# Kernel optimization log

Hardware: AMD Instinct MI355X
Metric: run time of the kernel (lower is better)

## Reference

```python
import jax, jax.numpy as jnp
import numpy as np

EMBED_DIM = 512
NUM_HEADS = 8
HEAD_DIM = EMBED_DIM // NUM_HEADS
SCALING = HEAD_DIM ** -0.5
T, B = 2048, 4
NEG_INF = -1e9


def setup_inputs() -> dict:
    key = jax.random.key(0)
    k1, k2, k3 = jax.random.split(key, 3)
    h = jax.random.normal(k1, (T, B, EMBED_DIM), dtype=jnp.float32)
    # causal additive mask, [T, T]: 0 on/below diagonal, -inf above
    attn_mask = jnp.where(jnp.triu(jnp.ones((T, T), dtype=bool), k=1), NEG_INF, 0.0).astype(jnp.float32)
    in_proj_weight = jax.random.normal(k2, (3 * EMBED_DIM, EMBED_DIM), dtype=jnp.float32) * 0.02
    in_proj_bias = jnp.zeros((3 * EMBED_DIM,), dtype=jnp.float32)
    out_w = jax.random.normal(k3, (EMBED_DIM, EMBED_DIM), dtype=jnp.float32) * 0.02
    out_b = jnp.zeros((EMBED_DIM,), dtype=jnp.float32)
    return {"h": h, "attn_mask": attn_mask, "in_proj_weight": in_proj_weight,
            "in_proj_bias": in_proj_bias, "out_w": out_w, "out_b": out_b}


def reference(h, attn_mask, in_proj_weight, in_proj_bias, out_w, out_b):
    tgt_len, bsz, embed_dim = h.shape
    # fused QKV projection: [T, B, 3E]
    qkv = jnp.einsum('tbe,fe->tbf', h, in_proj_weight) + in_proj_bias
    q, k, v = jnp.split(qkv, 3, axis=-1)
    q = q * SCALING
    # [T, B, E] -> [B*H, T, hd]
    def to_heads(x):
        return x.reshape(tgt_len, bsz * NUM_HEADS, HEAD_DIM).transpose(1, 0, 2)
    q, k, v = to_heads(q), to_heads(k), to_heads(v)
    # scores: [B*H, T, S]
    attn_weights = jnp.einsum('bth,bsh->bts', q, k)
    attn_weights = attn_weights + attn_mask[None, :, :]
    attn_p = jax.nn.softmax(attn_weights, axis=-1)
    attn = jnp.einsum('bts,bsh->bth', attn_p, v)
    # [B*H, T, hd] -> [T, B, E]
    attn = attn.transpose(1, 0, 2).reshape(tgt_len, bsz, embed_dim)
    out = jnp.einsum('tbe,fe->tbf', attn, out_w) + out_b
    return out, attn_p.reshape(bsz, NUM_HEADS, tgt_len, tgt_len)
```

## Files before the change

kernel.cpp:

```cpp
#include <hip/hip_runtime.h>
#include <cstdint>
#include <cstddef>

#define T_SEQ 2048
#define BSZ 4
#define EMB 512
#define NH 8
#define HD 64
#define SCALING 0.125f
#define NEGBIG (-1e30f)
#define PW 144

typedef short bf16x8_t __attribute__((ext_vector_type(8)));
typedef float f32x4_t __attribute__((ext_vector_type(4)));
typedef short short4v __attribute__((ext_vector_type(4)));
typedef float float4v __attribute__((ext_vector_type(4)));

typedef __attribute__((address_space(1))) const void* as1_cvp;
typedef __attribute__((address_space(3))) void* as3_vp;

#define MFMA16(a, b, c) __builtin_amdgcn_mfma_f32_16x16x32_bf16((a), (b), (c), 0, 0, 0)

static __device__ __forceinline__ short f2b(float f) {
  union { float f; uint32_t u; } x; x.f = f;
  uint32_t r = (x.u + 0x7fffu + ((x.u >> 16) & 1u)) >> 16;
  return (short)(r & 0xffffu);
}

static __device__ __forceinline__ void gload_lds16(const void* g, void* l) {
  __builtin_amdgcn_global_load_lds((as1_cvp)g, (as3_vp)l, 16, 0, 0);
}

__global__ __launch_bounds__(256) void cvt_kernel(const float* __restrict__ in,
                                                  short* __restrict__ out) {
  int i = (blockIdx.x * 256 + threadIdx.x) * 4;
  float4v v = *(const float4v*)(in + i);
  short4v o;
  o[0] = f2b(v[0]); o[1] = f2b(v[1]); o[2] = f2b(v[2]); o[3] = f2b(v[3]);
  *(short4v*)(out + i) = o;
}

template <int EPI>
__global__ __launch_bounds__(256)
void gemm_bt(const short* __restrict__ A, const short* __restrict__ Bt,
             const float* __restrict__ bias,
             short* __restrict__ outQ, short* __restrict__ outK, short* __restrict__ outV,
             float* __restrict__ outF, float* __restrict__ Pfill) {
  __shared__ short ldsA[128 * 32];
  __shared__ short ldsB[128 * 32];
  const int tid = threadIdx.x;
  const int wid = tid >> 6, lane = tid & 63, g = lane >> 4, r16 = lane & 15;
  const int wr = wid >> 1, wc = wid & 1;
  const int mbase = blockIdx.y * 128, nbase = blockIdx.x * 128;

  f32x4_t acc[4][4];
#pragma unroll
  for (int m = 0; m < 4; ++m)
#pragma unroll
    for (int n = 0; n < 4; ++n) acc[m][n] = (f32x4_t){0.f, 0.f, 0.f, 0.f};

  for (int kt = 0; kt < 16; ++kt) {
    __syncthreads();
#pragma unroll
    for (int i = 0; i < 2; ++i) {
      int c = i * 256 + tid;
      int row = c >> 2, j4 = c & 3;
      gload_lds16(A + (size_t)(mbase + row) * 512 + kt * 32 + j4 * 8, &ldsA[c * 8]);
      gload_lds16(Bt + (size_t)(nbase + row) * 512 + kt * 32 + j4 * 8, &ldsB[c * 8]);
    }
    __syncthreads();
    bf16x8_t af[4], bfv[4];
#pragma unroll
    for (int m = 0; m < 4; ++m)
      af[m] = *(const bf16x8_t*)&ldsA[(wr * 64 + m * 16 + r16) * 32 + g * 8];
#pragma unroll
    for (int n = 0; n < 4; ++n)
      bfv[n] = *(const bf16x8_t*)&ldsB[(wc * 64 + n * 16 + r16) * 32 + g * 8];
#pragma unroll
    for (int m = 0; m < 4; ++m)
#pragma unroll
      for (int n = 0; n < 4; ++n) acc[m][n] = MFMA16(af[m], bfv[n], acc[m][n]);
  }

#pragma unroll
  for (int m = 0; m < 4; ++m) {
#pragma unroll
    for (int n = 0; n < 4; ++n) {
      int col = nbase + wc * 64 + n * 16 + r16;
      float bcol = bias[col];
#pragma unroll
      for (int j = 0; j < 4; ++j) {
        int row = mbase + wr * 64 + m * 16 + g * 4 + j;
        float v = acc[m][n][j] + bcol;
        if (EPI == 0) {
          int sect = col >> 9, e = col & 511, hh = e >> 6, d = e & 63;
          int t = row >> 2, b = row & 3;
          size_t dst = ((size_t)(b * NH + hh) * T_SEQ + t) * HD + d;
          short bv = f2b(v);
          if (sect == 0) outQ[dst] = bv;
          else if (sect == 1) outK[dst] = bv;
          else outV[dst] = bv;
        } else {
          outF[(size_t)row * EMB + col] = v;
        }
      }
    }
  }

  if (EPI == 0) {
    const int bid = blockIdx.y * gridDim.x + blockIdx.x;
    const int nblk = gridDim.x * gridDim.y;
    const float4v z = {0.f, 0.f, 0.f, 0.f};
    for (int pair = bid; pair < 1024; pair += nblk) {
      const int qt = pair >> 5, bh = pair & 31;
      const int c0 = (qt + 1) * 64;
      const int nf4 = (T_SEQ - c0) >> 2;
      if (nf4 <= 0) continue;
      float* base = Pfill + ((size_t)bh * T_SEQ + qt * 64) * T_SEQ + c0;
      for (int r = 0; r < 64; ++r) {
        float* rowp = base + (size_t)r * T_SEQ;
        for (int c = tid; c < nf4; c += 256)
          __builtin_nontemporal_store(z, (float4v*)(rowp + c * 4));
      }
    }
  }
}

__global__ __launch_bounds__(256)
void attn_fused(const short* __restrict__ Qg, const short* __restrict__ Kg,
                const short* __restrict__ Vg, float* __restrict__ Pout,
                short* __restrict__ attnO) {
  __shared__ __align__(16) short lds[26624];
  short* Kt = lds;
  short* Vt = lds + 8192;
  short(*Pl)[16 * PW] = (short(*)[16 * PW])(lds + 8192 + 9216);
  const int bh = blockIdx.x;
  const int qt = 31 - (int)blockIdx.y;
  const int tid = threadIdx.x, wid = tid >> 6, lane = tid & 63;
  const int g = lane >> 4, r16 = lane & 15;
  const size_t headOff = (size_t)bh * T_SEQ * HD;
  const int wrow0 = qt * 64 + wid * 16;
  const int myrow = wrow0 + r16;
  const int maxcol = qt * 64 + 64;
  const int nt128 = (qt >> 1) + 1;
  const short* Kh = Kg + headOff;
  const short* Vh = Vg + headOff;

  bf16x8_t qf[2];
  {
    const short* qp = Qg + headOff + (size_t)myrow * HD + g * 8;
    qf[0] = *(const bf16x8_t*)qp;
    qf[1] = *(const bf16x8_t*)(qp + 32);
  }

  float m_w = NEGBIG;
  float m_t = NEGBIG;
  float l_w = 0.f;
  f32x4_t oacc[4];
#pragma unroll
  for (int dc = 0; dc < 4; ++dc) oacc[dc] = (f32x4_t){0.f, 0.f, 0.f, 0.f};

  uint32_t* Vtu = (uint32_t*)Vt;
  const int kp0 = tid & 63, dg0 = tid >> 6;

  bf16x8_t va[2], vb[2];
#define VLOAD(KB)                                                              \
  {                                                                            \
    const short* vp0 = Vh + (size_t)((KB) + kp0 * 2) * HD + dg0 * 8;           \
    va[0] = *(const bf16x8_t*)vp0; vb[0] = *(const bf16x8_t*)(vp0 + HD);       \
    const short* vp1 = vp0 + 32;                                               \
    va[1] = *(const bf16x8_t*)vp1; vb[1] = *(const bf16x8_t*)(vp1 + HD);       \
  }
  VLOAD(0)

  for (int kt = 0; kt < nt128; ++kt) {
    const int kb = kt * 128;
    __syncthreads();
#pragma unroll
    for (int i = 0; i < 4; ++i) {
      int cc = i * 256 + tid;
      int row = cc >> 3, j8 = (cc & 7) ^ (row & 7);
      gload_lds16(Kh + (size_t)(kb + row) * HD + j8 * 8, &Kt[cc * 8]);
    }
#pragma unroll
    for (int i = 0; i < 2; ++i) {
      int dg = dg0 + i * 4;
#pragma unroll
      for (int j = 0; j < 8; ++j)
        Vtu[(dg * 8 + j) * (PW / 2) + kp0] =
            (uint32_t)(uint16_t)va[i][j] | ((uint32_t)(uint16_t)vb[i][j] << 16);
    }
    __syncthreads();
    if (kt + 1 < nt128) VLOAD(kb + 128)
    const int H = ((maxcol - kb) >= 128) ? 2 : 1;
#pragma unroll
    for (int h = 0; h < 2; ++h) {
      if (h < H) {
        float sv[4][4];
#pragma unroll
        for (int kc4 = 0; kc4 < 4; ++kc4) {
          const int rl = (h * 4 + kc4) * 16 + r16;
          f32x4_t s = {0.f, 0.f, 0.f, 0.f};
#pragma unroll
          for (int kk = 0; kk < 2; ++kk) {
            int byteo = (rl * 128 + kk * 64 + g * 16) ^ ((rl & 7) << 4);
            bf16x8_t kf = *(const bf16x8_t*)((const char*)Kt + byteo);
            s = MFMA16(kf, qf[kk], s);
          }
          const int key0 = kb + (h * 4 + kc4) * 16 + g * 4;
#pragma unroll
          for (int j = 0; j < 4; ++j)
            sv[kc4][j] = (key0 + j <= myrow) ? s[j] * SCALING : NEGBIG;
        }
        float pm = NEGBIG;
#pragma unroll
        for (int kc4 = 0; kc4 < 4; ++kc4)
#pragma unroll
          for (int j = 0; j < 4; ++j) pm = fmaxf(pm, sv[kc4][j]);
        m_t = fmaxf(m_t, pm);
#pragma unroll
        for (int off = 1; off < 64; off <<= 1) pm = fmaxf(pm, __shfl_xor(pm, off));
        float mn = fmaxf(m_w, pm);
        if (mn > m_w + 8.f) {
          float sc = __expf(m_w - mn);
          l_w *= sc;
#pragma unroll
          for (int dc = 0; dc < 4; ++dc)
#pragma unroll
            for (int j = 0; j < 4; ++j) oacc[dc][j] *= sc;
          m_w = mn;
        }
#pragma unroll
        for (int kc4 = 0; kc4 < 4; ++kc4) {
          short4v pb;
#pragma unroll
          for (int j = 0; j < 4; ++j) {
            float e = __expf(sv[kc4][j] - m_w);
            l_w += e;
            pb[j] = f2b(e);
          }
          *(short4v*)&Pl[wid][r16 * PW + (h * 4 + kc4) * 16 + g * 4] = pb;
        }
#pragma unroll
        for (int kk2 = 0; kk2 < 2; ++kk2) {
          const int kc2 = h * 2 + kk2;
          bf16x8_t pf = *(const bf16x8_t*)&Pl[wid][r16 * PW + kc2 * 32 + g * 8];
#pragma unroll
          for (int dc = 0; dc < 4; ++dc) {
            bf16x8_t vf = *(const bf16x8_t*)&Vt[(dc * 16 + r16) * PW + kc2 * 32 + g * 8];
            oacc[dc] = MFMA16(pf, vf, oacc[dc]);
          }
        }
      }
    }
  }

#pragma unroll
  for (int off = 16; off <= 32; off <<= 1) {
    m_t = fmaxf(m_t, __shfl_xor(m_t, off));
    l_w += __shfl_xor(l_w, off);
  }
  const float m_row = m_t;
  const float rl2 = __expf(m_row - m_w) / l_w;

  float lo[4];
#pragma unroll
  for (int j = 0; j < 4; ++j) lo[j] = 1.0f / __shfl(l_w, g * 4 + j);
#pragma unroll
  for (int dc = 0; dc < 4; ++dc) {
#pragma unroll
    for (int j = 0; j < 4; ++j) {
      int t = wrow0 + g * 4 + j, d = dc * 16 + r16;
      size_t ntok = (size_t)t * BSZ + (bh >> 3);
      attnO[ntok * EMB + (bh & 7) * HD + d] = f2b(oacc[dc][j] * lo[j]);
    }
  }

  short* Kb0 = lds;
  short* Kb1 = lds + 8192;
  float* Prow = Pout + ((size_t)bh * T_SEQ + myrow) * T_SEQ;

#define STAGEK(KB, BUF)                                                        \
  {                                                                            \
    _Pragma("unroll")                                                          \
    for (int i = 0; i < 4; ++i) {                                              \
      int cc = i * 256 + tid;                                                  \
      int row = cc >> 3, j8 = (cc & 7) ^ (row & 7);                            \
      gload_lds16(Kh + (size_t)((KB) + row) * HD + j8 * 8, &(BUF)[cc * 8]);    \
    }                                                                          \
  }

  __syncthreads();
  STAGEK(0, Kb0)
  __syncthreads();
  int p = 0;
  for (int kt = 0; kt < nt128; ++kt) {
    const int kb = kt * 128;
    short* cur = p ? Kb1 : Kb0;
    short* nxt = p ? Kb0 : Kb1;
    if (kt + 1 < nt128) STAGEK(kb + 128, nxt)
    const int navail = (maxcol - kb) >> 4;
    const int nkc = navail < 8 ? navail : 8;
#pragma unroll
    for (int kc = 0; kc < 8; ++kc) {
      if (kc < nkc) {
        const int rl = kc * 16 + r16;
        f32x4_t s = {0.f, 0.f, 0.f, 0.f};
#pragma unroll
        for (int kk = 0; kk < 2; ++kk) {
          int byteo = (rl * 128 + kk * 64 + g * 16) ^ ((rl & 7) << 4);
          bf16x8_t kf = *(const bf16x8_t*)((const char*)cur + byteo);
          s = MFMA16(kf, qf[kk], s);
        }
        const int key0 = kb + kc * 16 + g * 4;
        float4v pvv;
#pragma unroll
        for (int j = 0; j < 4; ++j) {
          float e = __expf(s[j] * SCALING - m_row) * rl2;
          pvv[j] = (key0 + j <= myrow) ? e : 0.f;
        }
        *(float4v*)(Prow + key0) = pvv;
      }
    }
    __syncthreads();
    p ^= 1;
  }
}

extern "C" void kernel_launch(void* const* d_in, const int* in_sizes, int n_in,
                              void* d_out, int out_size, void* d_ws, size_t ws_size,
                              hipStream_t stream) {
  const float* h = (const float*)d_in[0];
  const float* w_in = (const float*)d_in[2];
  const float* b_in = (const float*)d_in[3];
  const float* w_out = (const float*)d_in[4];
  const float* b_out = (const float*)d_in[5];
  float* out = (float*)d_out;
  float* Pout = out + (size_t)T_SEQ * BSZ * EMB;

  short* hB = (short*)d_ws;
  short* wB = hB + (size_t)8192 * 512;
  short* owB = wB + (size_t)1536 * 512;
  short* qB = owB + (size_t)512 * 512;
  short* kB = qB + (size_t)32 * 2048 * 64;
  short* vB = kB + (size_t)32 * 2048 * 64;
  short* aB = vB + (size_t)32 * 2048 * 64;

  cvt_kernel<<<4096, 256, 0, stream>>>(h, hB);
  cvt_kernel<<<768, 256, 0, stream>>>(w_in, wB);
  cvt_kernel<<<256, 256, 0, stream>>>(w_out, owB);

  gemm_bt<0><<<dim3(12, 64), 256, 0, stream>>>(hB, wB, b_in, qB, kB, vB, nullptr, Pout);
  attn_fused<<<dim3(32, 32), 256, 0, stream>>>(qB, kB, vB, Pout, aB);
  gemm_bt<1><<<dim3(4, 64), 256, 0, stream>>>(aB, owB, b_out, nullptr, nullptr, nullptr, out, nullptr);
}
```

Measured before the change: 233.8 us.

## Write unnormalized probabilities in first pass and rescale instead of recomputing scores

The second pass that recomputed QK^T from restaged K tiles is removed. The first pass now writes the unnormalized exp values straight to the probability output and records the running max for each 64-key chunk in shared memory. A final pass reads P back from global memory and rescales each chunk by exp(m_chunk - m_final)/l. This drops the K staging and score MFMAs of the second pass, but adds a full read and rewrite of the large fp32 P matrix, so whether it pays off depends on how much of that traffic stays in cache.

```diff
diff --git a/kernel.cpp b/kernel.cpp
--- a/kernel.cpp
+++ b/kernel.cpp
@@ -134,6 +134,7 @@
   short* Kt = lds;
   short* Vt = lds + 8192;
   short(*Pl)[16 * PW] = (short(*)[16 * PW])(lds + 8192 + 9216);
+  __shared__ float mwt[4][32];
   const int bh = blockIdx.x;
   const int qt = 31 - (int)blockIdx.y;
   const int tid = threadIdx.x, wid = tid >> 6, lane = tid & 63;
@@ -145,6 +146,7 @@
   const int nt128 = (qt >> 1) + 1;
   const short* Kh = Kg + headOff;
   const short* Vh = Vg + headOff;
+  float* Prow = Pout + ((size_t)bh * T_SEQ + myrow) * T_SEQ;
 
   bf16x8_t qf[2];
   {
@@ -154,7 +156,6 @@
   }
 
   float m_w = NEGBIG;
-  float m_t = NEGBIG;
   float l_w = 0.f;
   f32x4_t oacc[4];
 #pragma unroll
@@ -217,7 +218,6 @@
         for (int kc4 = 0; kc4 < 4; ++kc4)
 #pragma unroll
           for (int j = 0; j < 4; ++j) pm = fmaxf(pm, sv[kc4][j]);
-        m_t = fmaxf(m_t, pm);
 #pragma unroll
         for (int off = 1; off < 64; off <<= 1) pm = fmaxf(pm, __shfl_xor(pm, off));
         float mn = fmaxf(m_w, pm);
@@ -230,15 +230,20 @@
             for (int j = 0; j < 4; ++j) oacc[dc][j] *= sc;
           m_w = mn;
         }
+        if (lane == 0) mwt[wid][kt * 2 + h] = m_w;
 #pragma unroll
         for (int kc4 = 0; kc4 < 4; ++kc4) {
+          const int key0 = kb + (h * 4 + kc4) * 16 + g * 4;
           short4v pb;
+          float4v ev;
 #pragma unroll
           for (int j = 0; j < 4; ++j) {
             float e = __expf(sv[kc4][j] - m_w);
             l_w += e;
+            ev[j] = e;
             pb[j] = f2b(e);
           }
+          *(float4v*)(Prow + key0) = ev;
           *(short4v*)&Pl[wid][r16 * PW + (h * 4 + kc4) * 16 + g * 4] = pb;
         }
 #pragma unroll
@@ -256,12 +261,7 @@
   }
 
 #pragma unroll
-  for (int off = 16; off <= 32; off <<= 1) {
-    m_t = fmaxf(m_t, __shfl_xor(m_t, off));
-    l_w += __shfl_xor(l_w, off);
-  }
-  const float m_row = m_t;
-  const float rl2 = __expf(m_row - m_w) / l_w;
+  for (int off = 16; off <= 32; off <<= 1) l_w += __shfl_xor(l_w, off);
 
   float lo[4];
 #pragma unroll
@@ -276,54 +276,18 @@
     }
   }
 
-  short* Kb0 = lds;
-  short* Kb1 = lds + 8192;
-  float* Prow = Pout + ((size_t)bh * T_SEQ + myrow) * T_SEQ;
-
-#define STAGEK(KB, BUF)                                                        \
-  {                                                                            \
-    _Pragma("unroll")                                                          \
-    for (int i = 0; i < 4; ++i) {                                              \
-      int cc = i * 256 + tid;                                                  \
-      int row = cc >> 3, j8 = (cc & 7) ^ (row & 7);                            \
-      gload_lds16(Kh + (size_t)((KB) + row) * HD + j8 * 8, &(BUF)[cc * 8]);    \
-    }                                                                          \
-  }
-
-  __syncthreads();
-  STAGEK(0, Kb0)
-  __syncthreads();
-  int p = 0;
-  for (int kt = 0; kt < nt128; ++kt) {
-    const int kb = kt * 128;
-    short* cur = p ? Kb1 : Kb0;
-    short* nxt = p ? Kb0 : Kb1;
-    if (kt + 1 < nt128) STAGEK(kb + 128, nxt)
-    const int navail = (maxcol - kb) >> 4;
-    const int nkc = navail < 8 ? navail : 8;
-#pragma unroll
-    for (int kc = 0; kc < 8; ++kc) {
-      if (kc < nkc) {
-        const int rl = kc * 16 + r16;
-        f32x4_t s = {0.f, 0.f, 0.f, 0.f};
-#pragma unroll
-        for (int kk = 0; kk < 2; ++kk) {
-          int byteo = (rl * 128 + kk * 64 + g * 16) ^ ((rl & 7) << 4);
-          bf16x8_t kf = *(const bf16x8_t*)((const char*)cur + byteo);
-          s = MFMA16(kf, qf[kk], s);
-        }
-        const int key0 = kb + kc * 16 + g * 4;
-        float4v pvv;
-#pragma unroll
-        for (int j = 0; j < 4; ++j) {
-          float e = __expf(s[j] * SCALING - m_row) * rl2;
-          pvv[j] = (key0 + j <= myrow) ? e : 0.f;
-        }
-        *(float4v*)(Prow + key0) = pvv;
-      }
-    }
-    __syncthreads();
-    p ^= 1;
+  const float inv_l = 1.0f / l_w;
+  asm volatile("s_waitcnt vmcnt(0)" ::: "memory");
+  const int nh2 = maxcol >> 6;
+  for (int h2 = 0; h2 < nh2; ++h2) {
+    const float f = __expf(mwt[wid][h2] - m_w) * inv_l;
+    const int c0 = h2 * 64 + g * 16;
+#pragma unroll
+    for (int j4 = 0; j4 < 4; ++j4) {
+      float4v v = *(const float4v*)(Prow + c0 + j4 * 4);
+      v[0] *= f; v[1] *= f; v[2] *= f; v[3] *= f;
+      *(float4v*)(Prow + c0 + j4 * 4) = v;
+    }
   }
 }
 
```

After: 329.1 us. 1.41x slower.
